# Kernel optimization log

Hardware: AMD Instinct MI355X
Metric: run time of the kernel (lower is better)

## Reference

```python
import jax, jax.numpy as jnp
import numpy as np

B, CIN, COUT, H, W = 4, 64, 64, 192, 192
KS, N, EPS = 3, 9, 1e-5


def setup_inputs() -> dict:
    key = jax.random.key(0)
    ks = jax.random.split(key, 4)
    return {
        "inputs": jax.random.normal(ks[0], (B, CIN, H, W), jnp.float32),
        "w_p": jax.random.normal(ks[1], (2 * N, CIN, KS, KS), jnp.float32) * 0.01,
        "b_p": jnp.zeros((2 * N,), jnp.float32),
        "w_m": jax.random.normal(ks[2], (N, CIN, KS, KS), jnp.float32) * 0.05,
        "b_m": jnp.zeros((N,), jnp.float32),
        "w_conv": jax.random.normal(ks[3], (COUT, CIN, KS, KS), jnp.float32) * (1.0 / np.sqrt(CIN * N)),
        "gamma": jnp.ones((COUT,), jnp.float32),
        "beta": jnp.zeros((COUT,), jnp.float32),
    }


def _conv3x3(x, w, b):
    y = jax.lax.conv_general_dilated(x, w, (1, 1), ((1, 1), (1, 1)),
                                     dimension_numbers=("NCHW", "OIHW", "NCHW"))
    return y + b[None, :, None, None]


def reference(inputs, w_p, b_p, w_m, b_m, w_conv, gamma, beta):
    x = inputs
    b, c, h, w = x.shape
    offset = _conv3x3(x, w_p, b_p)                 # (B, 2N, H, W)
    m = jax.nn.sigmoid(_conv3x3(x, w_m, b_m))      # (B, N, H, W)

    xp = jnp.pad(x, ((0, 0), (0, 0), (1, 1), (1, 1)))  # zero pad by 1
    hp, wp = h + 2, w + 2

    off = offset.transpose(0, 2, 3, 1)             # (B, H, W, 2N), first N=y, last N=x
    ky, kx = jnp.meshgrid(jnp.arange(-1, 2), jnp.arange(-1, 2), indexing="ij")
    pny = ky.reshape(-1).astype(x.dtype)           # (N,) kernel dy, ky-major order
    pnx = kx.reshape(-1).astype(x.dtype)
    p0y = jnp.arange(1, h + 1, dtype=x.dtype)      # base coords in padded image
    p0x = jnp.arange(1, w + 1, dtype=x.dtype)

    py = p0y[None, :, None, None] + pny + off[..., :N]   # (B, H, W, N)
    px = p0x[None, None, :, None] + pnx + off[..., N:]

    qy0 = jnp.clip(jnp.floor(py), 0, hp - 1)
    qy1 = jnp.clip(jnp.floor(py) + 1, 0, hp - 1)
    qx0 = jnp.clip(jnp.floor(px), 0, wp - 1)
    qx1 = jnp.clip(jnp.floor(px) + 1, 0, wp - 1)
    pyc = jnp.clip(py, 0, hp - 1)
    pxc = jnp.clip(px, 0, wp - 1)

    g_lt = (1 + (qy0 - pyc)) * (1 + (qx0 - pxc))
    g_rb = (1 - (qy1 - pyc)) * (1 - (qx1 - pxc))
    g_lb = (1 + (qy0 - pyc)) * (1 - (qx1 - pxc))
    g_rt = (1 - (qy1 - pyc)) * (1 + (qx0 - pxc))

    xf = xp.reshape(b, c, hp * wp)

    def gather(qy, qx):
        idx = (qy.astype(jnp.int32) * wp + qx.astype(jnp.int32)).reshape(b, 1, -1)
        idx = jnp.broadcast_to(idx, (b, c, idx.shape[-1]))
        return jnp.take_along_axis(xf, idx, axis=2).reshape(b, c, h, w, N)

    x_s = (g_lt[:, None] * gather(qy0, qx0)
           + g_rb[:, None] * gather(qy1, qx1)
           + g_lb[:, None] * gather(qy0, qx1)
           + g_rt[:, None] * gather(qy1, qx0))          # (B, C, H, W, N)
    x_s = x_s * m.transpose(0, 2, 3, 1)[:, None]        # modulation (B,1,H,W,N)

    # main conv over the 9 sampled taps (== conv with stride=ks on rearranged tensor)
    out = jnp.einsum("bchwn,ocn->bohw", x_s, w_conv.reshape(w_conv.shape[0], c, N))

    # BatchNorm2d (training mode: batch stats), ReLU, MaxPool(2)
    mu = out.mean((0, 2, 3), keepdims=True)
    var = ((out - mu) ** 2).mean((0, 2, 3), keepdims=True)
    out = gamma[None, :, None, None] * (out - mu) * jax.lax.rsqrt(var + EPS) + beta[None, :, None, None]
    out = jax.nn.relu(out)
    bo, co, ho, wo = out.shape
    out = out.reshape(bo, co, ho // 2, 2, wo // 2, 2).max(axis=(3, 5))
    return out
```

## Files before the change

kernel.cpp:

```cpp
#include <hip/hip_runtime.h>
#include <hip/hip_bf16.h>
#include <math.h>

#define HW     192
#define PLANE  (HW*HW)
#define CIN    64
#define COUT   64
#define NB     4
#define NPIX   (NB*PLANE)
#define H2     194
#define W2     200
#define WR     7
#define WC     24
#define NPOS   (WR*WC)

typedef __attribute__((ext_vector_type(8))) short bf16x8;
typedef __attribute__((ext_vector_type(4))) float f32x4;

static __device__ __forceinline__ ushort f2bf(float f) {
    __hip_bfloat16 h = __float2bfloat16(f);
    return __builtin_bit_cast(ushort, h);
}
static __device__ __forceinline__ float bf2f(ushort u) {
    return __builtin_bit_cast(float, ((unsigned)u) << 16);
}

__global__ __launch_bounds__(256) void kpadprep(
    const float* __restrict__ x,
    const float* __restrict__ wc, const float* __restrict__ w_p,
    const float* __restrict__ w_m,
    ushort* __restrict__ xt, ushort* __restrict__ wbf, ushort* __restrict__ womf)
{
    int blk = blockIdx.x;
    int t   = threadIdx.x;
    if (blk < NB * H2) {
        __shared__ ushort sT[W2 * 72];
        int b = blk / H2, y = blk % H2;
        const float* xb = x + (size_t)b * CIN * PLANE;
        bool yok = (y >= 1 && y <= HW);
#pragma unroll
        for (int it = 0; it < 25; ++it) {
            int idx = t + 256 * it;
            int cp  = (idx * 5243) >> 20;
            int col = idx - cp * 200;
            int c   = cp * 2;
            float v0 = 0.f, v1 = 0.f;
            if (yok && col >= 1 && col <= HW) {
                const float* s0 = xb + (size_t)c * PLANE + (y - 1) * HW + (col - 1);
                v0 = s0[0]; v1 = s0[PLANE];
            }
            *(unsigned*)&sT[col * 72 + c] =
                (unsigned)f2bf(v0) | ((unsigned)f2bf(v1) << 16);
        }
        __syncthreads();
        uint4* dst = (uint4*)(xt + ((size_t)(b * H2 + y) * W2) * 64);
#pragma unroll
        for (int it = 0; it < 7; ++it) {
            int idx = t + 256 * it;
            if (idx < 1600) {
                int col = idx >> 3, g = idx & 7;
                dst[idx] = *(uint4*)&sT[col * 72 + g * 8];
            }
        }
        return;
    }
    int i = (blk - NB * H2) * 256 + t;
    if (i < 4608) {
        int lane  = i & 63;
        int rc    = i >> 6;
        int chunk = rc % 18;
        int og    = rc / 18;
        int o  = og * 16 + (lane & 15);
        int k0 = chunk * 32 + (lane >> 4) * 8;
        ushort v[8];
#pragma unroll
        for (int j = 0; j < 8; ++j) {
            int k = k0 + j, c = k & 63, n = k >> 6;
            v[j] = f2bf(wc[o * 576 + c * 9 + n]);
        }
        ((uint4*)wbf)[i] = *(uint4*)v;
    } else if (i < 6912) {
        int ii    = i - 4608;
        int lane  = ii & 63;
        int rc    = ii >> 6;
        int chunk = rc % 18;
        int og    = rc / 18;
        int co = og * 16 + (lane & 15);
        int k0 = chunk * 32 + (lane >> 4) * 8;
        ushort v[8];
#pragma unroll
        for (int j = 0; j < 8; ++j) {
            int k = k0 + j, c = k & 63, n = k >> 6;
            float w = 0.f;
            if (co < 18)      w = w_p[(co * 64 + c) * 9 + n];
            else if (co < 27) w = w_m[((co - 18) * 64 + c) * 9 + n];
            v[j] = f2bf(w);
        }
        ((uint4*)womf)[ii] = *(uint4*)v;
    }
}

__global__ __launch_bounds__(256, 4) void kdeform(
    const ushort* __restrict__ xt,
    const ushort* __restrict__ wbf, const ushort* __restrict__ womf,
    const float* __restrict__ b_p, const float* __restrict__ b_m,
    ushort* __restrict__ outp)
{
    __shared__ ushort sWin[NPOS * 64];
    __shared__ ushort sXF[9216];
    __shared__ float4 sG[9][16];
    __shared__ uint   sPos[9][16];
    __shared__ uint   sOg[9][16];
    __shared__ float  sOM[32][17];
    __shared__ int    sFlag;

    int t    = threadIdx.x;
    int pix0 = blockIdx.x * 16;
    int b    = pix0 / PLANE;
    int rem  = pix0 - b * PLANE;
    int h    = rem / HW;
    int w0   = rem - h * HW;
    int rbase = min(max(h - 2, 0), H2 - WR);
    int wbase = min(max(w0 - 2, 0), 196 - WC);
    if (t == 0) sFlag = 0;

    const ushort* xtb = xt + (size_t)(b * H2) * W2 * 64;

    {
        const uint4* gsrc = (const uint4*)(xtb + ((size_t)rbase * W2 + wbase) * 64);
#pragma unroll
        for (int it = 0; it < 6; ++it) {
            int idx = t + 256 * it;
            if (idx < NPOS * 8) {
                int pos = idx >> 3, s = idx & 7;
                int g   = (s - pos) & 7;
                int r   = (pos * 2731) >> 16;
                int cc  = pos - r * WC;
                *(uint4*)&sWin[pos * 64 + s * 8] = gsrc[((r * W2 + cc) << 3) + g];
            }
        }
    }
    __syncthreads();

    if (t < 128) {
        int lane = t & 63, og = t >> 6;
        int sub  = lane >> 4;
        int hr   = h - rbase;
        int wrp  = w0 - wbase + (lane & 15);
        f32x4 acc = {0.f, 0.f, 0.f, 0.f};
#pragma unroll
        for (int chunk = 0; chunk < 18; ++chunk) {
            bf16x8 a = *(const bf16x8*)&womf[((og * 18 + chunk) * 64 + lane) * 8];
            int n  = chunk >> 1;
            int dy = n / 3, dx = n - dy * 3;
            int pos  = (hr + dy) * WC + wrp + dx;
            int slot = ((chunk & 1) * 4 + sub + pos) & 7;
            bf16x8 bb = *(const bf16x8*)&sWin[pos * 64 + slot * 8];
            acc = __builtin_amdgcn_mfma_f32_16x16x32_bf16(a, bb, acc, 0, 0, 0);
        }
        int col = lane & 15, row0 = sub * 4;
#pragma unroll
        for (int r = 0; r < 4; ++r) sOM[og * 16 + row0 + r][col] = acc[r];
    }
    __syncthreads();

    if (t < 144) {
        int pp = t & 15, n = t >> 4;
        float offy = sOM[n][pp]      + b_p[n];
        float offx = sOM[9 + n][pp]  + b_p[9 + n];
        float mr   = sOM[18 + n][pp] + b_m[n];
        float m = 1.f / (1.f + __expf(-mr));
        int dy = n / 3, dx = n - dy * 3;
        float py = (float)(h + dy) + offy;
        float px = (float)(w0 + pp + dx) + offx;
        float fy = floorf(py), fx = floorf(px);
        float qy0 = fminf(fmaxf(fy,       0.f), 193.f);
        float qy1 = fminf(fmaxf(fy + 1.f, 0.f), 193.f);
        float qx0 = fminf(fmaxf(fx,       0.f), 193.f);
        float qx1 = fminf(fmaxf(fx + 1.f, 0.f), 193.f);
        float pyc = fminf(fmaxf(py, 0.f), 193.f);
        float pxc = fminf(fmaxf(px, 0.f), 193.f);
        float ay = 1.f + qy0 - pyc, by = 1.f - (qy1 - pyc);
        float ax = 1.f + qx0 - pxc, bx = 1.f - (qx1 - pxc);
        int ry0 = (int)qy0, ry1 = (int)qy1;
        int cx0 = (int)qx0, cx1 = (int)qx1;
        int xs  = cx1 - cx0;
        sOg[n][pp] = (uint)(ry0 | (ry1 << 8) | (cx0 << 16) | (xs << 24));
        int p00 = (ry0 - rbase) * WC + (cx0 - wbase);
        int p10 = (ry1 - rbase) * WC + (cx0 - wbase);
        sPos[n][pp] = (uint)((p00 & 255) | (((p00 + xs) & 255) << 8)
                           | ((p10 & 255) << 16) | (((p10 + xs) & 255) << 24));
        sG[n][pp] = make_float4(ay * ax * m, ay * bx * m, by * ax * m, by * bx * m);
        if (ry0 < rbase || ry1 > rbase + (WR - 1) ||
            cx0 < wbase || cx1 > wbase + (WC - 1))
            atomicOr(&sFlag, 1);
    }
    __syncthreads();

    {
        int px  = t & 15, sub = t >> 4;
        int o8  = sub & 7;
        bool fb = (sFlag != 0);
#pragma unroll
        for (int it = 0; it < 5; ++it) {
            int item = sub + 16 * it;
            if (item >= 72) break;
            int n = item >> 3;
            float4 G = sG[n][px];
            bf16x8 a0, a1, c0, c1;
            if (!fb) {
                uint pk = sPos[n][px];
                int p00 = pk & 255, p01 = (pk >> 8) & 255;
                int p10 = (pk >> 16) & 255, p11 = pk >> 24;
                a0 = *(const bf16x8*)&sWin[p00 * 64 + ((o8 + p00) & 7) * 8];
                a1 = *(const bf16x8*)&sWin[p01 * 64 + ((o8 + p01) & 7) * 8];
                c0 = *(const bf16x8*)&sWin[p10 * 64 + ((o8 + p10) & 7) * 8];
                c1 = *(const bf16x8*)&sWin[p11 * 64 + ((o8 + p11) & 7) * 8];
            } else {
                uint gp = sOg[n][px];
                int ry0 = gp & 255, ry1 = (gp >> 8) & 255;
                int cx0 = (gp >> 16) & 255, xs = gp >> 24;
                const ushort* g0 = xtb + (size_t)(ry0 * W2 + cx0) * 64 + o8 * 8;
                const ushort* g1 = xtb + (size_t)(ry1 * W2 + cx0) * 64 + o8 * 8;
                a0 = *(const bf16x8*)g0;
                a1 = *(const bf16x8*)(g0 + xs * 64);
                c0 = *(const bf16x8*)g1;
                c1 = *(const bf16x8*)(g1 + xs * 64);
            }
            ushort pk8[8] __attribute__((aligned(16)));
#pragma unroll
            for (int j = 0; j < 8; ++j) {
                float v = G.x * bf2f((ushort)a0[j]) + G.y * bf2f((ushort)a1[j])
                        + G.z * bf2f((ushort)c0[j]) + G.w * bf2f((ushort)c1[j]);
                pk8[j] = f2bf(v);
            }
            int chunk = n * 2 + (o8 >> 2), s16 = o8 & 3;
            *(uint4*)&sXF[(chunk * 64 + s16 * 16 + (px ^ s16)) * 8] = *(uint4*)pk8;
        }
    }
    __syncthreads();

    {
        int lane = t & 63, og = t >> 6;
        int sub = lane >> 4, pcol = lane & 15;
        f32x4 acc = {0.f, 0.f, 0.f, 0.f};
#pragma unroll
        for (int chunk = 0; chunk < 18; ++chunk) {
            bf16x8 a  = *(const bf16x8*)&wbf[((og * 18 + chunk) * 64 + lane) * 8];
            bf16x8 bb = *(const bf16x8*)&sXF[(chunk * 64 + sub * 16 + (pcol ^ sub)) * 8];
            acc = __builtin_amdgcn_mfma_f32_16x16x32_bf16(a, bb, acc, 0, 0, 0);
        }
        int row0 = sub * 4;
        ushort* ob = outp + ((size_t)(b * COUT + og * 16 + row0)) * PLANE + rem + pcol;
        ob[0]                 = f2bf(acc[0]);
        ob[(size_t)PLANE]     = f2bf(acc[1]);
        ob[2 * (size_t)PLANE] = f2bf(acc[2]);
        ob[3 * (size_t)PLANE] = f2bf(acc[3]);
    }
}

__global__ __launch_bounds__(256) void kstats(
    const ushort* __restrict__ outp, float* __restrict__ partial)
{
    int o  = blockIdx.x >> 3;
    int sl = blockIdx.x & 7;
    int t  = threadIdx.x;
    float s = 0.f, s2 = 0.f;
    for (int b = 0; b < NB; ++b) {
        const uint4* pl = (const uint4*)(outp + ((size_t)(b * COUT + o)) * PLANE
                                         + sl * (PLANE / 8));
        for (int i = t; i < PLANE / 64; i += 256) {
            uint4 v = pl[i];
            unsigned ua[4] = {v.x, v.y, v.z, v.w};
#pragma unroll
            for (int j = 0; j < 4; ++j) {
                float lo = __builtin_bit_cast(float, ua[j] << 16);
                float hi = __builtin_bit_cast(float, ua[j] & 0xffff0000u);
                s  += lo + hi;
                s2 += lo * lo + hi * hi;
            }
        }
    }
    __shared__ float rs[256], rs2[256];
    rs[t] = s; rs2[t] = s2;
    __syncthreads();
    for (int st = 128; st > 0; st >>= 1) {
        if (t < st) { rs[t] += rs[t + st]; rs2[t] += rs2[t + st]; }
        __syncthreads();
    }
    if (t == 0) {
        partial[o * 8 + sl]       = rs[0];
        partial[512 + o * 8 + sl] = rs2[0];
    }
}

__global__ __launch_bounds__(256) void kbnpool(
    const ushort* __restrict__ outp, const float* __restrict__ partial,
    const float* __restrict__ gamma, const float* __restrict__ beta,
    float* __restrict__ out)
{
    int i = blockIdx.x * 256 + threadIdx.x;
    int wo  = i % 96;
    int tmp = i / 96;
    int ho  = tmp % 96; tmp /= 96;
    int o   = tmp % 64;
    int b   = tmp / 64;
    float s = 0.f, s2 = 0.f;
#pragma unroll
    for (int sl = 0; sl < 8; ++sl) {
        s  += partial[o * 8 + sl];
        s2 += partial[512 + o * 8 + sl];
    }
    float inv  = 1.f / (float)(NB * PLANE);
    float mean = s * inv;
    float var  = s2 * inv - mean * mean;
    float rsq  = rsqrtf(var + 1e-5f);
    float g  = gamma[o] * rsq;
    float bt = beta[o] - mean * g;
    const ushort* pl = outp + ((size_t)(b * COUT + o)) * PLANE + (2 * ho) * HW + 2 * wo;
    unsigned u01 = *(const unsigned*)pl;
    unsigned u23 = *(const unsigned*)(pl + HW);
    float y00 = fmaxf(g * bf2f((ushort)(u01 & 0xffff)) + bt, 0.f);
    float y01 = fmaxf(g * bf2f((ushort)(u01 >> 16))    + bt, 0.f);
    float y10 = fmaxf(g * bf2f((ushort)(u23 & 0xffff)) + bt, 0.f);
    float y11 = fmaxf(g * bf2f((ushort)(u23 >> 16))    + bt, 0.f);
    out[i] = fmaxf(fmaxf(y00, y01), fmaxf(y10, y11));
}

extern "C" void kernel_launch(void* const* d_in, const int* in_sizes, int n_in,
                              void* d_out, int out_size, void* d_ws, size_t ws_size,
                              hipStream_t stream)
{
    const float* x      = (const float*)d_in[0];
    const float* w_p    = (const float*)d_in[1];
    const float* b_p    = (const float*)d_in[2];
    const float* w_m    = (const float*)d_in[3];
    const float* b_m    = (const float*)d_in[4];
    const float* w_conv = (const float*)d_in[5];
    const float* gamma  = (const float*)d_in[6];
    const float* beta   = (const float*)d_in[7];
    float* out = (float*)d_out;

    char* ws = (char*)d_ws;
    ushort* xt      = (ushort*)ws;
    ushort* outp    = (ushort*)(ws + 19865600);
    float*  partial = (float*)(ws + 38739968);
    ushort* wbf     = (ushort*)(ws + 38744064);
    ushort* womf    = (ushort*)(ws + 38817792);

    kpadprep<<<NB * H2 + 27, 256, 0, stream>>>(x, w_conv, w_p, w_m, xt, wbf, womf);
    kdeform<<<NPIX / 16, 256, 0, stream>>>(xt, wbf, womf, b_p, b_m, outp);
    kstats<<<512, 256, 0, stream>>>(outp, partial);
    kbnpool<<<(NB * COUT * 96 * 96) / 256, 256, 0, stream>>>(outp, partial, gamma, beta, out);
}
```

Baseline: 192.1 us.

## Shrink deform window, alias shared buffers, split pad-prep rows, pack bf16 unpack

Narrows the per-block input window from 24 to 21 columns and overlays the offset-conv result buffer onto the sampled-feature buffer in one manually laid out shared array, cutting LDS per block so more blocks can be resident. The sampling coefficients are now held in registers and written after an extra barrier, because they would otherwise overwrite the aliased region still being read. The pad/transpose kernel is split into two half-row blocks per row for more parallelism, and the bilinear interpolation unpacks bf16 pairs into float2 vectors. The narrower window may push more blocks onto the slow global-memory fallback path.

Result: faster. 181.9 us (-5.3%).

```diff
diff --git a/kernel.cpp b/kernel.cpp
--- a/kernel.cpp
+++ b/kernel.cpp
@@ -11,11 +11,12 @@
 #define H2     194
 #define W2     200
 #define WR     7
-#define WC     24
+#define WC     21
 #define NPOS   (WR*WC)
 
 typedef __attribute__((ext_vector_type(8))) short bf16x8;
 typedef __attribute__((ext_vector_type(4))) float f32x4;
+typedef __attribute__((ext_vector_type(2))) float f32x2;
 
 static __device__ __forceinline__ ushort f2bf(float f) {
     __hip_bfloat16 h = __float2bfloat16(f);
@@ -23,6 +24,12 @@
 }
 static __device__ __forceinline__ float bf2f(ushort u) {
     return __builtin_bit_cast(float, ((unsigned)u) << 16);
+}
+static __device__ __forceinline__ f32x2 up2(unsigned u) {
+    f32x2 r;
+    r.x = __builtin_bit_cast(float, u << 16);
+    r.y = __builtin_bit_cast(float, u & 0xffff0000u);
+    return r;
 }
 
 __global__ __launch_bounds__(256) void kpadprep(
@@ -33,38 +40,44 @@
 {
     int blk = blockIdx.x;
     int t   = threadIdx.x;
-    if (blk < NB * H2) {
-        __shared__ ushort sT[W2 * 72];
-        int b = blk / H2, y = blk % H2;
+    if (blk < NB * H2 * 2) {
+        __shared__ ushort sT[100 * 72];
+        int half = blk & 1;
+        int y    = (blk >> 1) % H2;
+        int b    = (blk >> 1) / H2;
+        int col0 = half * 100;
         const float* xb = x + (size_t)b * CIN * PLANE;
         bool yok = (y >= 1 && y <= HW);
 #pragma unroll
-        for (int it = 0; it < 25; ++it) {
+        for (int it = 0; it < 13; ++it) {
             int idx = t + 256 * it;
-            int cp  = (idx * 5243) >> 20;
-            int col = idx - cp * 200;
-            int c   = cp * 2;
-            float v0 = 0.f, v1 = 0.f;
-            if (yok && col >= 1 && col <= HW) {
-                const float* s0 = xb + (size_t)c * PLANE + (y - 1) * HW + (col - 1);
-                v0 = s0[0]; v1 = s0[PLANE];
-            }
-            *(unsigned*)&sT[col * 72 + c] =
-                (unsigned)f2bf(v0) | ((unsigned)f2bf(v1) << 16);
+            if (idx < 3200) {
+                int cp   = (idx * 5243) >> 19;
+                int lcol = idx - cp * 100;
+                int col  = col0 + lcol;
+                int c    = cp * 2;
+                float v0 = 0.f, v1 = 0.f;
+                if (yok && col >= 1 && col <= HW) {
+                    const float* s0 = xb + (size_t)c * PLANE + (y - 1) * HW + (col - 1);
+                    v0 = s0[0]; v1 = s0[PLANE];
+                }
+                *(unsigned*)&sT[lcol * 72 + c] =
+                    (unsigned)f2bf(v0) | ((unsigned)f2bf(v1) << 16);
+            }
         }
         __syncthreads();
         uint4* dst = (uint4*)(xt + ((size_t)(b * H2 + y) * W2) * 64);
 #pragma unroll
-        for (int it = 0; it < 7; ++it) {
+        for (int it = 0; it < 4; ++it) {
             int idx = t + 256 * it;
-            if (idx < 1600) {
-                int col = idx >> 3, g = idx & 7;
-                dst[idx] = *(uint4*)&sT[col * 72 + g * 8];
+            if (idx < 800) {
+                int lcol = idx >> 3, g = idx & 7;
+                dst[(col0 + lcol) * 8 + g] = *(uint4*)&sT[lcol * 72 + g * 8];
             }
         }
         return;
     }
-    int i = (blk - NB * H2) * 256 + t;
+    int i = (blk - NB * H2 * 2) * 256 + t;
     if (i < 4608) {
         int lane  = i & 63;
         int rc    = i >> 6;
@@ -106,13 +119,14 @@
     const float* __restrict__ b_p, const float* __restrict__ b_m,
     ushort* __restrict__ outp)
 {
-    __shared__ ushort sWin[NPOS * 64];
-    __shared__ ushort sXF[9216];
-    __shared__ float4 sG[9][16];
-    __shared__ uint   sPos[9][16];
-    __shared__ uint   sOg[9][16];
-    __shared__ float  sOM[32][17];
-    __shared__ int    sFlag;
+    __shared__ __align__(16) char smem[40708];
+    ushort* sWin = (ushort*)smem;
+    ushort* sXF  = (ushort*)(smem + 18816);
+    float (*sOM)[17] = (float(*)[17])(smem + 18816);
+    float4 (*sG)[16] = (float4(*)[16])(smem + 37248);
+    uint (*sPos)[16] = (uint(*)[16])(smem + 39552);
+    uint (*sOg)[16]  = (uint(*)[16])(smem + 40128);
+    int* sFlag = (int*)(smem + 40704);
 
     int t    = threadIdx.x;
     int pix0 = blockIdx.x * 16;
@@ -121,20 +135,20 @@
     int h    = rem / HW;
     int w0   = rem - h * HW;
     int rbase = min(max(h - 2, 0), H2 - WR);
-    int wbase = min(max(w0 - 2, 0), 196 - WC);
-    if (t == 0) sFlag = 0;
+    int wbase = min(max(w0 - 2, 0), W2 - WC - 4);
+    if (t == 0) *sFlag = 0;
 
     const ushort* xtb = xt + (size_t)(b * H2) * W2 * 64;
 
     {
         const uint4* gsrc = (const uint4*)(xtb + ((size_t)rbase * W2 + wbase) * 64);
 #pragma unroll
-        for (int it = 0; it < 6; ++it) {
+        for (int it = 0; it < 5; ++it) {
             int idx = t + 256 * it;
             if (idx < NPOS * 8) {
                 int pos = idx >> 3, s = idx & 7;
                 int g   = (s - pos) & 7;
-                int r   = (pos * 2731) >> 16;
+                int r   = (pos * 3121) >> 16;
                 int cc  = pos - r * WC;
                 *(uint4*)&sWin[pos * 64 + s * 8] = gsrc[((r * W2 + cc) << 3) + g];
             }
@@ -164,6 +178,7 @@
     }
     __syncthreads();
 
+    uint pkC = 0, ogC = 0; float4 gC;
     if (t < 144) {
         int pp = t & 15, n = t >> 4;
         float offy = sOM[n][pp]      + b_p[n];
@@ -185,54 +200,66 @@
         int ry0 = (int)qy0, ry1 = (int)qy1;
         int cx0 = (int)qx0, cx1 = (int)qx1;
         int xs  = cx1 - cx0;
-        sOg[n][pp] = (uint)(ry0 | (ry1 << 8) | (cx0 << 16) | (xs << 24));
+        ogC = (uint)(ry0 | (ry1 << 8) | (cx0 << 16) | (xs << 24));
         int p00 = (ry0 - rbase) * WC + (cx0 - wbase);
         int p10 = (ry1 - rbase) * WC + (cx0 - wbase);
-        sPos[n][pp] = (uint)((p00 & 255) | (((p00 + xs) & 255) << 8)
-                           | ((p10 & 255) << 16) | (((p10 + xs) & 255) << 24));
-        sG[n][pp] = make_float4(ay * ax * m, ay * bx * m, by * ax * m, by * bx * m);
+        pkC = (uint)((p00 & 255) | (((p00 + xs) & 255) << 8)
+                   | ((p10 & 255) << 16) | (((p10 + xs) & 255) << 24));
+        gC = make_float4(ay * ax * m, ay * bx * m, by * ax * m, by * bx * m);
         if (ry0 < rbase || ry1 > rbase + (WR - 1) ||
             cx0 < wbase || cx1 > wbase + (WC - 1))
-            atomicOr(&sFlag, 1);
+            atomicOr(sFlag, 1);
+    }
+    __syncthreads();
+    if (t < 144) {
+        int pp = t & 15, n = t >> 4;
+        sOg[n][pp]  = ogC;
+        sPos[n][pp] = pkC;
+        sG[n][pp]   = gC;
     }
     __syncthreads();
 
     {
         int px  = t & 15, sub = t >> 4;
         int o8  = sub & 7;
-        bool fb = (sFlag != 0);
+        bool fb = (*sFlag != 0);
 #pragma unroll
         for (int it = 0; it < 5; ++it) {
             int item = sub + 16 * it;
             if (item >= 72) break;
             int n = item >> 3;
             float4 G = sG[n][px];
-            bf16x8 a0, a1, c0, c1;
+            uint4 A0, A1, C0, C1;
             if (!fb) {
                 uint pk = sPos[n][px];
                 int p00 = pk & 255, p01 = (pk >> 8) & 255;
                 int p10 = (pk >> 16) & 255, p11 = pk >> 24;
-                a0 = *(const bf16x8*)&sWin[p00 * 64 + ((o8 + p00) & 7) * 8];
-                a1 = *(const bf16x8*)&sWin[p01 * 64 + ((o8 + p01) & 7) * 8];
-                c0 = *(const bf16x8*)&sWin[p10 * 64 + ((o8 + p10) & 7) * 8];
-                c1 = *(const bf16x8*)&sWin[p11 * 64 + ((o8 + p11) & 7) * 8];
+                A0 = *(const uint4*)&sWin[p00 * 64 + ((o8 + p00) & 7) * 8];
+                A1 = *(const uint4*)&sWin[p01 * 64 + ((o8 + p01) & 7) * 8];
+                C0 = *(const uint4*)&sWin[p10 * 64 + ((o8 + p10) & 7) * 8];
+                C1 = *(const uint4*)&sWin[p11 * 64 + ((o8 + p11) & 7) * 8];
             } else {
                 uint gp = sOg[n][px];
                 int ry0 = gp & 255, ry1 = (gp >> 8) & 255;
                 int cx0 = (gp >> 16) & 255, xs = gp >> 24;
                 const ushort* g0 = xtb + (size_t)(ry0 * W2 + cx0) * 64 + o8 * 8;
                 const ushort* g1 = xtb + (size_t)(ry1 * W2 + cx0) * 64 + o8 * 8;
-                a0 = *(const bf16x8*)g0;
-                a1 = *(const bf16x8*)(g0 + xs * 64);
-                c0 = *(const bf16x8*)g1;
-                c1 = *(const bf16x8*)(g1 + xs * 64);
-            }
+                A0 = *(const uint4*)g0;
+                A1 = *(const uint4*)(g0 + xs * 64);
+                C0 = *(const uint4*)g1;
+                C1 = *(const uint4*)(g1 + xs * 64);
+            }
+            unsigned ua0[4] = {A0.x, A0.y, A0.z, A0.w};
+            unsigned ua1[4] = {A1.x, A1.y, A1.z, A1.w};
+            unsigned uc0[4] = {C0.x, C0.y, C0.z, C0.w};
+            unsigned uc1[4] = {C1.x, C1.y, C1.z, C1.w};
             ushort pk8[8] __attribute__((aligned(16)));
 #pragma unroll
-            for (int j = 0; j < 8; ++j) {
-                float v = G.x * bf2f((ushort)a0[j]) + G.y * bf2f((ushort)a1[j])
-                        + G.z * bf2f((ushort)c0[j]) + G.w * bf2f((ushort)c1[j]);
-                pk8[j] = f2bf(v);
+            for (int q = 0; q < 4; ++q) {
+                f32x2 v = G.x * up2(ua0[q]) + G.y * up2(ua1[q])
+                        + G.z * up2(uc0[q]) + G.w * up2(uc1[q]);
+                pk8[2 * q]     = f2bf(v.x);
+                pk8[2 * q + 1] = f2bf(v.y);
             }
             int chunk = n * 2 + (o8 >> 2), s16 = o8 & 3;
             *(uint4*)&sXF[(chunk * 64 + s16 * 16 + (px ^ s16)) * 8] = *(uint4*)pk8;
@@ -348,7 +375,7 @@
     ushort* wbf     = (ushort*)(ws + 38744064);
     ushort* womf    = (ushort*)(ws + 38817792);
 
-    kpadprep<<<NB * H2 + 27, 256, 0, stream>>>(x, w_conv, w_p, w_m, xt, wbf, womf);
+    kpadprep<<<NB * H2 * 2 + 27, 256, 0, stream>>>(x, w_conv, w_p, w_m, xt, wbf, womf);
     kdeform<<<NPIX / 16, 256, 0, stream>>>(xt, wbf, womf, b_p, b_m, outp);
     kstats<<<512, 256, 0, stream>>>(outp, partial);
     kbnpool<<<(NB * COUT * 96 * 96) / 256, 256, 0, stream>>>(outp, partial, gamma, beta, out);
```
